# Kernel tuning notes

Hardware: AMD Instinct MI355X
Metric: run time of the kernel (lower is better)

The kernel has to match this reference:

```python
import jax, jax.numpy as jnp
import numpy as np

B, S, D, H = 2, 512, 1024, 8
DK = D // H
DFF = 4 * D
R = 51
SEP = 64


def setup_inputs() -> dict:
    key = jax.random.key(0)
    ks = jax.random.split(key, 12)
    def w(k, shape, scale=0.02):
        return jax.random.normal(k, shape, jnp.float32) * scale
    return {
        "x": jax.random.normal(ks[0], (B, S, D), jnp.float32),
        "relation": jax.random.randint(ks[1], (B, S, S), 0, R),
        "mask": jnp.ones((B, S, S), jnp.int32),
        "sep_id": SEP,
        "history_reg": jnp.ones((1,), jnp.float32),
        "Wq": w(ks[2], (D, D)), "bq": jnp.zeros((D,), jnp.float32),
        "Wk": w(ks[3], (D, D)), "bk": jnp.zeros((D,), jnp.float32),
        "Wv": w(ks[4], (D, D)), "bv": jnp.zeros((D,), jnp.float32),
        "Wo": w(ks[5], (D, D)), "bo": jnp.zeros((D,), jnp.float32),
        "rel_k_emb": w(ks[6], (R, DK)),
        "rel_v_emb": w(ks[7], (R, DK)),
        "ln1_g": jnp.ones((D,), jnp.float32), "ln1_b": jnp.zeros((D,), jnp.float32),
        "ln2_g": jnp.ones((D,), jnp.float32), "ln2_b": jnp.zeros((D,), jnp.float32),
        "W1": w(ks[8], (D, DFF)), "b1": jnp.zeros((DFF,), jnp.float32),
        "W2": w(ks[9], (DFF, D)), "b2": jnp.zeros((D,), jnp.float32),
    }


def _layer_norm(x, g, b, eps=1e-5):
    m = jnp.mean(x, axis=-1, keepdims=True)
    v = jnp.mean(jnp.square(x - m), axis=-1, keepdims=True)
    return (x - m) * jax.lax.rsqrt(v + eps) * g + b


def _forward(x, relation, mask, sep_id, history_reg, Wq, bq, Wk, bk, Wv, bv, Wo, bo,
             rel_k_emb, rel_v_emb, ln1_g, ln1_b, ln2_g, ln2_b, W1, b1, W2, b2):
    b, s, d = x.shape
    # relation-aware self-attention sublayer (pre-norm)
    h = _layer_norm(x, ln1_g, ln1_b)
    rk = rel_k_emb[relation]  # [B,S,S,DK]
    rv = rel_v_emb[relation]  # [B,S,S,DK]
    def proj(W, bias):
        return (h @ W + bias).reshape(b, s, H, DK).transpose(0, 2, 1, 3)  # [B,H,S,DK]
    q, k, v = proj(Wq, bq), proj(Wk, bk), proj(Wv, bv)
    scores = jnp.einsum("bhid,bhjd->bhij", q, k) + jnp.einsum("bhid,bijd->bhij", q, rk)
    scores = scores / jnp.sqrt(jnp.float32(DK))
    scores = jnp.where(mask[:, None, :, :] == 0, jnp.float32(-1e9), scores)
    attn = jax.nn.softmax(scores, axis=-1)  # [B,H,S,S]
    ctx = jnp.einsum("bhij,bhjd->bhid", attn, v) + jnp.einsum("bhij,bijd->bhid", attn, rv)
    ctx = ctx.transpose(0, 2, 1, 3).reshape(b, s, d)
    attn_out = ctx @ Wo + bo
    # history regularization loss: attention mass on history tokens (positions < sep_id)
    loss = history_reg[0] * jnp.mean(attn[:, :, :, :sep_id])
    x = x + attn_out
    # FFN sublayer (pre-norm)
    h2 = _layer_norm(x, ln2_g, ln2_b)
    ffn = jax.nn.relu(h2 @ W1 + b1) @ W2 + b2
    x = x + ffn
    return x, loss


def reference(x, relation, mask, sep_id, history_reg, Wq, bq, Wk, bk, Wv, bv, Wo, bo,
              rel_k_emb, rel_v_emb, ln1_g, ln1_b, ln2_g, ln2_b, W1, b1, W2, b2):
    return _forward(x, relation, mask, sep_id, history_reg, Wq, bq, Wk, bk, Wv, bv,
                    Wo, bo, rel_k_emb, rel_v_emb, ln1_g, ln1_b, ln2_g, ln2_b,
                    W1, b1, W2, b2)
```

## Files before the change

### kernel.cpp

```cpp
#include <hip/hip_runtime.h>
#include <hip/hip_bf16.h>

#define NB 2
#define NS 512
#define ND 1024
#define NH 8
#define NDK 128
#define NDFF 4096
#define RPAD 64
#define LDSC 640
#define BSROWS 1024
#define NBH 16

typedef __bf16 bf16x8 __attribute__((ext_vector_type(8)));
typedef __bf16 bf16x4 __attribute__((ext_vector_type(4)));
typedef float f32x4 __attribute__((ext_vector_type(4)));

#define BM 64
#define BN 64
#define BK 64

__device__ __forceinline__ void gload16(const void* g, void* l) {
    __builtin_amdgcn_global_load_lds(
        (const __attribute__((address_space(1))) void*)g,
        (__attribute__((address_space(3))) void*)l, 16, 0, 0);
}

__global__ __launch_bounds__(256, 4) void gemm64(
    const __bf16* __restrict__ A, const __bf16* __restrict__ Bt,
    const __bf16* __restrict__ Brel, __bf16* __restrict__ vt,
    const __bf16* __restrict__ arP, const __bf16* __restrict__ rvP,
    __bf16* __restrict__ ctxmP,
    float* __restrict__ Cf, __bf16* __restrict__ Cb,
    const float* __restrict__ bias,
    int Ksp, int lda, int ldb, int ldc,
    long sA, long sA2, int zdivA,
    long sB, long sB2, int zdivB,
    long sC, int nsplit, long sPart, int flags)
{
    __shared__ __bf16 As0[BM * BK];
    __shared__ __bf16 As1[BM * BK];
    __shared__ __bf16 Bs0[BN * BK];
    __shared__ __bf16 Bs1[BN * BK];

    const unsigned gx = gridDim.x, gy = gridDim.y;
    const unsigned n = gx * gy * gridDim.z;
    const unsigned o = blockIdx.x + gx * (blockIdx.y + gy * blockIdx.z);
    const unsigned q = n >> 3, r = n & 7, xcd = o & 7;
    const unsigned nl = (xcd < r ? xcd * (q + 1) : r * (q + 1) + (xcd - r) * q) + (o >> 3);
    const unsigned bx = nl % gx, tmp = nl / gx;
    const unsigned by = tmp % gy, bz = tmp / gy;

    const int z = bz;
    const int bh = z / nsplit, sp = z - bh * nsplit;
    const long kbase = (long)sp * Ksp;
    A  += (long)(bh / zdivA) * sA + (long)(bh % zdivA) * sA2 + kbase;
    Bt += (long)(bh / zdivB) * sB + (long)(bh % zdivB) * sB2 + kbase;
    const long cbase = (long)bh * sC + (long)sp * sPart;

    const int tM = by * BM, tN = bx * BN;
    const int t = threadIdx.x, lane = t & 63, w = t >> 6;
    const int wr = w >> 1, wc = w & 1;

    const __bf16* Bbase = Bt;
    int ldbx = ldb, tNB = tN;
    if ((flags & 4) && tN >= NS) { Bbase = Brel + kbase; ldbx = 128; tNB = tN - NS; }

    const int srow = lane >> 3;
    const int scolE = ((((lane & 7) << 4) ^ (srow << 4)) >> 1);

    const __bf16* gA = A + (long)(tM + srow) * lda + scolE;
    const __bf16* gB = Bbase + (long)(tNB + srow) * ldbx + scolE;

    f32x4 acc[2][2];
#pragma unroll
    for (int m = 0; m < 2; ++m)
#pragma unroll
        for (int nn = 0; nn < 2; ++nn)
#pragma unroll
            for (int j = 0; j < 4; ++j) acc[m][nn][j] = 0.f;

    const int r16 = lane & 15;
    const int kq = (lane >> 4) * 8;
    const int xorE = (r16 & 7) * 8;
    const int nt = Ksp / BK;

    auto STAGE = [&](__bf16* as, __bf16* bs, int k0) {
#pragma unroll
        for (int i = 0; i < 2; ++i) {
            const int rr = (w + i * 4) * 8;
            gload16(gA + (long)rr * lda + k0, (void*)&as[rr * BK]);
            gload16(gB + (long)rr * ldbx + k0, (void*)&bs[rr * BK]);
        }
    };
    auto COMPUTE = [&](const __bf16* as, const __bf16* bs) {
        __builtin_amdgcn_s_setprio(1);
#pragma unroll
        for (int ks = 0; ks < 2; ++ks) {
            bf16x8 af[2], bv[2];
#pragma unroll
            for (int m = 0; m < 2; ++m)
                af[m] = *(const bf16x8*)&as[(wr * 32 + m * 16 + r16) * BK + ((ks * 32 + kq) ^ xorE)];
#pragma unroll
            for (int nn = 0; nn < 2; ++nn)
                bv[nn] = *(const bf16x8*)&bs[(wc * 32 + nn * 16 + r16) * BK + ((ks * 32 + kq) ^ xorE)];
#pragma unroll
            for (int m = 0; m < 2; ++m)
#pragma unroll
                for (int nn = 0; nn < 2; ++nn)
                    acc[m][nn] = __builtin_amdgcn_mfma_f32_16x16x32_bf16(af[m], bv[nn], acc[m][nn], 0, 0, 0);
        }
        __builtin_amdgcn_s_setprio(0);
    };

    STAGE(As0, Bs0, 0);
    STAGE(As1, Bs1, BK);
    for (int tt = 0; tt < nt; tt += 2) {
        asm volatile("s_waitcnt vmcnt(4)\n\ts_barrier" ::: "memory");
        COMPUTE(As0, Bs0);
        asm volatile("s_waitcnt lgkmcnt(0)\n\ts_barrier" ::: "memory");
        const bool more = (tt + 2 < nt);
        if (more) {
            STAGE(As0, Bs0, (tt + 2) * BK);
            asm volatile("s_waitcnt vmcnt(4)\n\ts_barrier" ::: "memory");
        } else {
            asm volatile("s_waitcnt vmcnt(0)\n\ts_barrier" ::: "memory");
        }
        COMPUTE(As1, Bs1);
        asm volatile("s_waitcnt lgkmcnt(0)\n\ts_barrier" ::: "memory");
        if (more) STAGE(As1, Bs1, (tt + 3) * BK);
    }

    if (flags & 16) {
        const int b = bh >> 3, h = bh & 7;
#pragma unroll
        for (int nn = 0; nn < 2; ++nn) {
            const int gc = tN + wc * 32 + nn * 16 + (lane & 15);
            bf16x8 rv[8];
#pragma unroll
            for (int qq = 0; qq < 8; ++qq)
                rv[qq] = ((const bf16x8*)&rvP[(long)gc * RPAD])[qq];
#pragma unroll
            for (int m = 0; m < 2; ++m) {
                const int gr0 = tM + wr * 32 + m * 16 + (lane >> 4) * 4;
#pragma unroll
                for (int j = 0; j < 4; ++j) {
                    const int row = gr0 + j;
                    const bf16x8* ar8 = (const bf16x8*)&arP[((long)bh * NS + row) * RPAD];
                    float d = 0.f;
#pragma unroll
                    for (int qq = 0; qq < 8; ++qq) {
                        const bf16x8 a = ar8[qq], vv = rv[qq];
#pragma unroll
                        for (int e = 0; e < 8; ++e) d += (float)a[e] * (float)vv[e];
                    }
                    ctxmP[((long)(b * NS + row)) * ND + h * NDK + gc] =
                        (__bf16)(acc[m][nn][j] + d);
                }
            }
        }
        return;
    }

    const bool relu = (flags & 1) != 0;
    const bool vmode = (flags & 8) && (tN >= 2 * ND);
#pragma unroll
    for (int m = 0; m < 2; ++m) {
        const int gr0 = tM + wr * 32 + m * 16 + (lane >> 4) * 4;
#pragma unroll
        for (int nn = 0; nn < 2; ++nn) {
            const int gc = tN + wc * 32 + nn * 16 + (lane & 15);
            const float bb = bias ? bias[gc] : 0.f;
            if (vmode) {
                const int hd = gc - 2 * ND;
                const int b = gr0 >> 9, i = gr0 & 511;
                bf16x4 ov;
#pragma unroll
                for (int j = 0; j < 4; ++j) ov[j] = (__bf16)(acc[m][nn][j] + bb);
                *(bf16x4*)&vt[(((long)b * NH + (hd >> 7)) * NDK + (hd & 127)) * NS + i] = ov;
            } else {
#pragma unroll
                for (int j = 0; j < 4; ++j) {
                    float v = acc[m][nn][j] + bb;
                    if (relu) v = fmaxf(v, 0.f);
                    const long idx = cbase + (long)(gr0 + j) * ldc + gc;
                    if (Cb) Cb[idx] = (__bf16)v;
                    else Cf[idx] = v;
                }
            }
        }
    }
}

__global__ void prep_weights(
    const float* __restrict__ Wq, const float* __restrict__ Wk,
    const float* __restrict__ Wv, const float* __restrict__ Wo,
    const float* __restrict__ W1, const float* __restrict__ W2,
    const float* __restrict__ relv,
    const float* __restrict__ bq, const float* __restrict__ bk,
    const float* __restrict__ bv, const float* __restrict__ relk,
    const float* __restrict__ x, const float* __restrict__ ln1g,
    const float* __restrict__ ln1b,
    __bf16* __restrict__ WqkvT, __bf16* __restrict__ WoT,
    __bf16* __restrict__ W1T, __bf16* __restrict__ W2T,
    __bf16* __restrict__ relvT, float* __restrict__ biasqkv,
    __bf16* __restrict__ relkT, __bf16* __restrict__ h1, int R)
{
    const int tile = blockIdx.x;
    const int t = threadIdx.y * 32 + threadIdx.x;

    if (tile >= 12372) {
        const long row = tile - 12372;
        const float* xr = x + row * ND;
        float4 v = reinterpret_cast<const float4*>(xr)[t];
        float s = v.x + v.y + v.z + v.w;
        float s2 = v.x * v.x + v.y * v.y + v.z * v.z + v.w * v.w;
#pragma unroll
        for (int o = 32; o > 0; o >>= 1) {
            s += __shfl_xor(s, o, 64);
            s2 += __shfl_xor(s2, o, 64);
        }
        __shared__ float red[8];
        const int lane = t & 63, wv = t >> 6;
        if (lane == 0) { red[wv] = s; red[4 + wv] = s2; }
        __syncthreads();
        s = red[0] + red[1] + red[2] + red[3];
        s2 = red[4] + red[5] + red[6] + red[7];
        const float mean = s * (1.f / ND);
        const float var = s2 * (1.f / ND) - mean * mean;
        const float rs = rsqrtf(var + 1e-5f);
        const float xv[4] = {v.x, v.y, v.z, v.w};
        bf16x4 o;
#pragma unroll
        for (int j = 0; j < 4; ++j) {
            const int c = t * 4 + j;
            o[j] = (__bf16)((xv[j] - mean) * rs * ln1g[c] + ln1b[c]);
        }
        *(bf16x4*)&h1[row * ND + t * 4] = o;
        return;
    }
    if (tile >= 12296) {
        const int ft = (tile - 12296) * 256 + t;
        if (ft < ND) biasqkv[ft] = bq[ft];
        else if (ft < 2 * ND) biasqkv[ft] = bk[ft - ND];
        else if (ft < 3 * ND) biasqkv[ft] = bv[ft - 2 * ND];
        else {
            const int idx = ft - 3 * ND;
            if (idx < 128 * NDK) {
                const int r = idx / NDK;
                relkT[idx] = (r < R) ? (__bf16)relk[idx] : (__bf16)0.f;
            }
        }
        return;
    }
    const float* src; __bf16* dst;
    int rows_in, cols_in, ldo, kx, ny;
    if (tile < 4096) {
        const int m = tile >> 10, r = tile & 1023;
        kx = r & 31; ny = r >> 5;
        rows_in = 1024; cols_in = 1024; ldo = 1024;
        src = m == 0 ? Wq : m == 1 ? Wk : m == 2 ? Wv : Wo;
        dst = m == 3 ? WoT : WqkvT + (size_t)m * 1024 * 1024;
    } else if (tile < 8192) {
        const int r = tile - 4096;
        kx = r & 31; ny = r >> 5;
        rows_in = 1024; cols_in = 4096; ldo = 1024; src = W1; dst = W1T;
    } else if (tile < 12288) {
        const int r = tile - 8192;
        kx = r & 127; ny = r >> 7;
        rows_in = 4096; cols_in = 1024; ldo = 4096; src = W2; dst = W2T;
    } else {
        const int r = tile - 12288;
        kx = r & 1; ny = r >> 1;
        rows_in = R; cols_in = 128; ldo = 64; src = relv; dst = relvT;
    }

    __shared__ float tl[32][33];
    const int k0 = kx * 32, n0 = ny * 32;
    const int tx = threadIdx.x, ty = threadIdx.y;
#pragma unroll
    for (int dy = 0; dy < 32; dy += 8) {
        const int k = k0 + ty + dy, nn = n0 + tx;
        tl[ty + dy][tx] = (k < rows_in && nn < cols_in) ? src[(long)k * cols_in + nn] : 0.f;
    }
    __syncthreads();
#pragma unroll
    for (int dy = 0; dy < 32; dy += 8) {
        const int nn = n0 + ty + dy, k = k0 + tx;
        if (nn < cols_in && k < ldo) dst[(long)nn * ldo + k] = (__bf16)tl[tx][ty + dy];
    }
}

__global__ __launch_bounds__(256) void softmax_rel(
    const __bf16* __restrict__ scores,
    const int* __restrict__ relation, const int* __restrict__ mask,
    __bf16* __restrict__ attn, __bf16* __restrict__ attnR,
    float* __restrict__ loss_part, const int* __restrict__ sep_p)
{
    const int i = blockIdx.x, b = blockIdx.y;
    const int t = threadIdx.x;
    const int* rrow = relation + ((long)b * NS + i) * NS;
    const int* mrow = mask + ((long)b * NS + i) * NS;
    const int r0 = rrow[t], r1 = rrow[t + 256];
    const int m0 = mrow[t], m1 = mrow[t + 256];
    const int sep = *sep_p;
    const int lane = t & 63, wv = t >> 6;

    __shared__ float qrl[RPAD];
    __shared__ float bins[RPAD];
    __shared__ float red[4];

    const float sc = 0.088388347648318447f;
    float lsum = 0.f;

#pragma unroll 1
    for (int h = 0; h < NH; ++h) {
        const long bh = (long)(b * NH + h);
        const __bf16* srow = scores + (bh * NS + i) * LDSC;
        __bf16* arow = attn + (bh * NS + i) * NS;
        __bf16* aRrow = attnR + (bh * NS + i) * RPAD;

        if (t < RPAD) { qrl[t] = (float)srow[NS + t]; bins[t] = 0.f; }
        __syncthreads();

        float v0 = ((float)srow[t] + qrl[r0]) * sc;
        float v1 = ((float)srow[t + 256] + qrl[r1]) * sc;
        if (m0 == 0) v0 = -1e9f;
        if (m1 == 0) v1 = -1e9f;

        float mx = fmaxf(v0, v1);
#pragma unroll
        for (int o = 32; o > 0; o >>= 1) mx = fmaxf(mx, __shfl_xor(mx, o, 64));
        if (lane == 0) red[wv] = mx;
        __syncthreads();
        mx = fmaxf(fmaxf(red[0], red[1]), fmaxf(red[2], red[3]));
        __syncthreads();

        const float e0 = __expf(v0 - mx), e1 = __expf(v1 - mx);
        float sm = e0 + e1;
#pragma unroll
        for (int o = 32; o > 0; o >>= 1) sm += __shfl_xor(sm, o, 64);
        if (lane == 0) red[wv] = sm;
        __syncthreads();
        sm = red[0] + red[1] + red[2] + red[3];

        const float inv = 1.f / sm;
        const float a0 = e0 * inv, a1 = e1 * inv;
        arow[t] = (__bf16)a0;
        arow[t + 256] = (__bf16)a1;
        atomicAdd(&bins[r0], a0);
        atomicAdd(&bins[r1], a1);
        if (t < sep) lsum += a0;
        if (t + 256 < sep) lsum += a1;
        __syncthreads();
        if (t < RPAD) aRrow[t] = (__bf16)bins[t];
        __syncthreads();
    }

#pragma unroll
    for (int o = 32; o > 0; o >>= 1) lsum += __shfl_xor(lsum, o, 64);
    if (lane == 0) red[wv] = lsum;
    __syncthreads();
    if (t == 0) loss_part[(long)b * NS + i] = red[0] + red[1] + red[2] + red[3];
}

__global__ __launch_bounds__(256) void wo_reduce_ln(
    const float* __restrict__ P, const float* __restrict__ x,
    const float* __restrict__ bo, const float* __restrict__ g,
    const float* __restrict__ bb, float* __restrict__ out,
    __bf16* __restrict__ h2)
{
    const int row = blockIdx.x;
    const int t = threadIdx.x;
    const long i4 = (long)row * 256 + t;
    const long sP = (long)BSROWS * ND / 4;
    const float4* P4 = (const float4*)P;
    float4 s = P4[i4];
    const float4 t1 = P4[i4 + sP];
    s.x += t1.x; s.y += t1.y; s.z += t1.z; s.w += t1.w;
    const int col = t * 4;
    const float4 xv = ((const float4*)x)[i4];
    const float4 bv = *(const float4*)&bo[col];
    float4 o;
    o.x = s.x + xv.x + bv.x; o.y = s.y + xv.y + bv.y;
    o.z = s.z + xv.z + bv.z; o.w = s.w + xv.w + bv.w;
    ((float4*)out)[i4] = o;

    float sum = o.x + o.y + o.z + o.w;
    float sum2 = o.x * o.x + o.y * o.y + o.z * o.z + o.w * o.w;
#pragma unroll
    for (int of = 32; of > 0; of >>= 1) {
        sum += __shfl_xor(sum, of, 64);
        sum2 += __shfl_xor(sum2, of, 64);
    }
    __shared__ float red[8];
    const int lane = t & 63, wv = t >> 6;
    if (lane == 0) { red[wv] = sum; red[4 + wv] = sum2; }
    __syncthreads();
    sum = red[0] + red[1] + red[2] + red[3];
    sum2 = red[4] + red[5] + red[6] + red[7];
    const float mean = sum * (1.f / ND);
    const float var = sum2 * (1.f / ND) - mean * mean;
    const float rs = rsqrtf(var + 1e-5f);
    const float ov[4] = {o.x, o.y, o.z, o.w};
    bf16x4 hb;
#pragma unroll
    for (int j = 0; j < 4; ++j)
        hb[j] = (__bf16)((ov[j] - mean) * rs * g[col + j] + bb[col + j]);
    *(bf16x4*)&h2[(long)row * ND + col] = hb;
}

__global__ __launch_bounds__(256) void ffn2_reduce(
    const float* __restrict__ P, const float* __restrict__ b2, float* __restrict__ out,
    const float* __restrict__ loss_part, const float* __restrict__ hist,
    const int* __restrict__ sep_p, float* __restrict__ out_loss)
{
    const int i4 = blockIdx.x * 256 + threadIdx.x;
    const long sP = (long)BSROWS * ND / 4;
    const float4* P4 = (const float4*)P;
    float4 s = P4[i4];
    const float4 t1 = P4[i4 + sP];
    s.x += t1.x; s.y += t1.y; s.z += t1.z; s.w += t1.w;
    const int col = (i4 * 4) & (ND - 1);
    const float4 bv = *(const float4*)&b2[col];
    float4 o = ((float4*)out)[i4];
    o.x += s.x + bv.x; o.y += s.y + bv.y;
    o.z += s.z + bv.z; o.w += s.w + bv.w;
    ((float4*)out)[i4] = o;

    if (blockIdx.x == 0) {
        const int t = threadIdx.x;
        const float4 v = ((const float4*)loss_part)[t];
        float ls = v.x + v.y + v.z + v.w;
#pragma unroll
        for (int of = 32; of > 0; of >>= 1) ls += __shfl_xor(ls, of, 64);
        __shared__ float red[4];
        if ((t & 63) == 0) red[t >> 6] = ls;
        __syncthreads();
        if (t == 0) {
            const int sep = *sep_p;
            const float total = red[0] + red[1] + red[2] + red[3];
            const float denom = (float)NB * NH * NS * (float)(sep > 0 ? sep : 1);
            out_loss[0] = (sep > 0) ? hist[0] * total / denom : 0.f;
        }
    }
}

static inline int cdiv(int a, int b) { return (a + b - 1) / b; }

extern "C" void kernel_launch(void* const* d_in, const int* in_sizes, int n_in,
                              void* d_out, int out_size, void* d_ws, size_t ws_size,
                              hipStream_t stream)
{
    const float* x      = (const float*)d_in[0];
    const int* relation = (const int*)d_in[1];
    const int* mask     = (const int*)d_in[2];
    const int* sep_p    = (const int*)d_in[3];
    const float* hist   = (const float*)d_in[4];
    const float* Wq = (const float*)d_in[5],  *bq = (const float*)d_in[6];
    const float* Wk = (const float*)d_in[7],  *bk = (const float*)d_in[8];
    const float* Wv = (const float*)d_in[9],  *bv = (const float*)d_in[10];
    const float* Wo = (const float*)d_in[11], *bo = (const float*)d_in[12];
    const float* relk = (const float*)d_in[13];
    const float* relv = (const float*)d_in[14];
    const float* ln1g = (const float*)d_in[15], *ln1b = (const float*)d_in[16];
    const float* ln2g = (const float*)d_in[17], *ln2b = (const float*)d_in[18];
    const float* W1 = (const float*)d_in[19], *b1 = (const float*)d_in[20];
    const float* W2 = (const float*)d_in[21], *b2 = (const float*)d_in[22];
    const int R = in_sizes[13] / NDK;

    float* out = (float*)d_out;
    float* out_loss = out + (long)BSROWS * ND;

    char* p = (char*)d_ws;
    auto alloc = [&](size_t bytes) -> void* {
        void* r = (void*)p;
        p += (bytes + 255) & ~(size_t)255;
        return r;
    };
    __bf16* WqkvT   = (__bf16*)alloc((size_t)3 * ND * ND * 2);
    __bf16* WoT     = (__bf16*)alloc((size_t)ND * ND * 2);
    __bf16* W1T     = (__bf16*)alloc((size_t)NDFF * ND * 2);
    __bf16* W2T     = (__bf16*)alloc((size_t)ND * NDFF * 2);
    __bf16* relkT   = (__bf16*)alloc((size_t)128 * NDK * 2);
    __bf16* relvT   = (__bf16*)alloc((size_t)NDK * RPAD * 2);
    float*  biasqkv = (float*)alloc((size_t)3 * ND * 4);
    __bf16* h1      = (__bf16*)alloc((size_t)BSROWS * ND * 2);
    __bf16* qkvb    = (__bf16*)alloc((size_t)BSROWS * 3 * ND * 2);
    __bf16* vt      = (__bf16*)alloc((size_t)NBH * NDK * NS * 2);
    __bf16* attnb   = (__bf16*)alloc((size_t)NBH * NS * NS * 2);
    __bf16* attnR   = (__bf16*)alloc((size_t)NBH * NS * RPAD * 2);
    __bf16* ctxm    = (__bf16*)alloc((size_t)BSROWS * ND * 2);
    __bf16* h2      = (__bf16*)alloc((size_t)BSROWS * ND * 2);
    __bf16* F1      = (__bf16*)alloc((size_t)BSROWS * NDFF * 2);
    float*  loss_part = (float*)alloc((size_t)NB * NS * 4);
    float*  arena   = (float*)alloc((size_t)64 * 1024 * 1024);
    __bf16* scoresb = (__bf16*)arena;
    float* woPart   = arena;
    float* f2Part   = arena + (size_t)2 * 1024 * 1024;

    const dim3 tb(32, 8);
    prep_weights<<<13396, tb, 0, stream>>>(Wq, Wk, Wv, Wo, W1, W2, relv,
                                           bq, bk, bv, relk, x, ln1g, ln1b,
                                           WqkvT, WoT, W1T, W2T, relvT,
                                           biasqkv, relkT, h1, R);

    gemm64<<<dim3(48, 16, 1), 256, 0, stream>>>(
        h1, WqkvT, nullptr, vt, nullptr, nullptr, nullptr,
        nullptr, qkvb, biasqkv,
        ND, ND, ND, 3 * ND,
        0, 0, 1, 0, 0, 1, 0, 1, 0, 8);

    gemm64<<<dim3(10, 8, NBH), 256, 0, stream>>>(
        qkvb, qkvb + ND, relkT, nullptr, nullptr, nullptr, nullptr,
        nullptr, scoresb, nullptr,
        NDK, 3 * ND, 3 * ND, LDSC,
        (long)NS * 3 * ND, NDK, NH,
        (long)NS * 3 * ND, NDK, NH,
        (long)NS * LDSC, 1, 0, 4);

    softmax_rel<<<dim3(NS, NB), 256, 0, stream>>>(
        scoresb, relation, mask, attnb, attnR, loss_part, sep_p);

    gemm64<<<dim3(2, 8, NBH), 256, 0, stream>>>(
        attnb, vt, nullptr, nullptr, attnR, relvT, ctxm,
        nullptr, nullptr, nullptr,
        NS, NS, NS, NDK,
        (long)NS * NS, 0, 1,
        (long)NDK * NS, 0, 1,
        0, 1, 0, 16);

    gemm64<<<dim3(16, 16, 2), 256, 0, stream>>>(
        ctxm, WoT, nullptr, nullptr, nullptr, nullptr, nullptr,
        woPart, nullptr, nullptr,
        512, ND, ND, ND,
        0, 0, 1, 0, 0, 1,
        0, 2, (long)BSROWS * ND, 0);

    wo_reduce_ln<<<BSROWS, 256, 0, stream>>>(woPart, x, bo, ln2g, ln2b, out, h2);

    gemm64<<<dim3(64, 16, 1), 256, 0, stream>>>(
        h2, W1T, nullptr, nullptr, nullptr, nullptr, nullptr,
        nullptr, F1, b1,
        ND, ND, ND, NDFF,
        0, 0, 1, 0, 0, 1, 0, 1, 0, 1);

    gemm64<<<dim3(16, 16, 2), 256, 0, stream>>>(
        F1, W2T, nullptr, nullptr, nullptr, nullptr, nullptr,
        f2Part, nullptr, nullptr,
        2048, NDFF, NDFF, ND,
        0, 0, 1, 0, 0, 1,
        0, 2, (long)BSROWS * ND, 0);

    ffn2_reduce<<<1024, 256, 0, stream>>>(f2Part, b2, out,
                                          loss_part, hist, sep_p, out_loss);
}
```

Baseline: 159.2 us.

## Fuse relation-aware attention into one kernel per 16-query tile

Replaces the three-kernel attention path (QK+relK scores GEMM, softmax_rel, attn·V GEMM with relV epilogue) with a single attn_fused kernel. Each block holds a 16-row score tile in LDS, computes QK^T and q·relK with MFMA, applies softmax with relation bins and the history loss, then multiplies by V and relV directly. This removes the global round-trips of the bf16 scores and attention matrices and two launches. In exchange each block carries a large LDS footprint, which limits occupancy, and V is read straight from global memory rather than staged through LDS.

```diff
diff --git a/kernel.cpp b/kernel.cpp
--- a/kernel.cpp
+++ b/kernel.cpp
@@ -8,9 +8,10 @@
 #define NDK 128
 #define NDFF 4096
 #define RPAD 64
-#define LDSC 640
 #define BSROWS 1024
 #define NBH 16
+#define QT 16
+#define SLP 524
 
 typedef __bf16 bf16x8 __attribute__((ext_vector_type(8)));
 typedef __bf16 bf16x4 __attribute__((ext_vector_type(4)));
@@ -28,9 +29,7 @@
 
 __global__ __launch_bounds__(256, 4) void gemm64(
     const __bf16* __restrict__ A, const __bf16* __restrict__ Bt,
-    const __bf16* __restrict__ Brel, __bf16* __restrict__ vt,
-    const __bf16* __restrict__ arP, const __bf16* __restrict__ rvP,
-    __bf16* __restrict__ ctxmP,
+    __bf16* __restrict__ vt,
     float* __restrict__ Cf, __bf16* __restrict__ Cb,
     const float* __restrict__ bias,
     int Ksp, int lda, int ldb, int ldc,
@@ -62,15 +61,11 @@
     const int t = threadIdx.x, lane = t & 63, w = t >> 6;
     const int wr = w >> 1, wc = w & 1;
 
-    const __bf16* Bbase = Bt;
-    int ldbx = ldb, tNB = tN;
-    if ((flags & 4) && tN >= NS) { Bbase = Brel + kbase; ldbx = 128; tNB = tN - NS; }
-
     const int srow = lane >> 3;
     const int scolE = ((((lane & 7) << 4) ^ (srow << 4)) >> 1);
 
     const __bf16* gA = A + (long)(tM + srow) * lda + scolE;
-    const __bf16* gB = Bbase + (long)(tNB + srow) * ldbx + scolE;
+    const __bf16* gB = Bt + (long)(tN + srow) * ldb + scolE;
 
     f32x4 acc[2][2];
 #pragma unroll
@@ -90,7 +85,7 @@
         for (int i = 0; i < 2; ++i) {
             const int rr = (w + i * 4) * 8;
             gload16(gA + (long)rr * lda + k0, (void*)&as[rr * BK]);
-            gload16(gB + (long)rr * ldbx + k0, (void*)&bs[rr * BK]);
+            gload16(gB + (long)rr * ldb + k0, (void*)&bs[rr * BK]);
         }
     };
     auto COMPUTE = [&](const __bf16* as, const __bf16* bs) {
@@ -131,37 +126,6 @@
         if (more) STAGE(As1, Bs1, (tt + 3) * BK);
     }
 
-    if (flags & 16) {
-        const int b = bh >> 3, h = bh & 7;
-#pragma unroll
-        for (int nn = 0; nn < 2; ++nn) {
-            const int gc = tN + wc * 32 + nn * 16 + (lane & 15);
-            bf16x8 rv[8];
-#pragma unroll
-            for (int qq = 0; qq < 8; ++qq)
-                rv[qq] = ((const bf16x8*)&rvP[(long)gc * RPAD])[qq];
-#pragma unroll
-            for (int m = 0; m < 2; ++m) {
-                const int gr0 = tM + wr * 32 + m * 16 + (lane >> 4) * 4;
-#pragma unroll
-                for (int j = 0; j < 4; ++j) {
-                    const int row = gr0 + j;
-                    const bf16x8* ar8 = (const bf16x8*)&arP[((long)bh * NS + row) * RPAD];
-                    float d = 0.f;
-#pragma unroll
-                    for (int qq = 0; qq < 8; ++qq) {
-                        const bf16x8 a = ar8[qq], vv = rv[qq];
-#pragma unroll
-                        for (int e = 0; e < 8; ++e) d += (float)a[e] * (float)vv[e];
-                    }
-                    ctxmP[((long)(b * NS + row)) * ND + h * NDK + gc] =
-                        (__bf16)(acc[m][nn][j] + d);
-                }
-            }
-        }
-        return;
-    }
-
     const bool relu = (flags & 1) != 0;
     const bool vmode = (flags & 8) && (tN >= 2 * ND);
 #pragma unroll
@@ -190,6 +154,180 @@
             }
         }
     }
+}
+
+__global__ __launch_bounds__(256, 2) void attn_fused(
+    const __bf16* __restrict__ qkvb, const __bf16* __restrict__ vt,
+    const __bf16* __restrict__ relkT, const __bf16* __restrict__ relvT,
+    const int* __restrict__ relation, const int* __restrict__ mask,
+    __bf16* __restrict__ ctxm, float* __restrict__ loss_part,
+    const int* __restrict__ sep_p)
+{
+    __shared__ float Sl[QT * SLP];
+    __shared__ __bf16 Ks0[64 * NDK];
+    __shared__ __bf16 Ks1[64 * NDK];
+    __shared__ float qrl[QT][RPAD];
+    __shared__ float bins[QT][68];
+    __shared__ float redl[4];
+
+    const unsigned o = blockIdx.x + 32u * blockIdx.y;
+    const unsigned nl = (o & 7) * 64u + (o >> 3);
+    const int qt = nl & 31, bh = nl >> 5;
+    const int b = bh >> 3, h = bh & 7;
+    const int i0 = qt * QT;
+
+    const int t = threadIdx.x, lane = t & 63, w = t >> 6;
+    const int r16 = lane & 15;
+    const int kq = (lane >> 4) * 8;
+    const int xorE = (r16 & 7) * 8;
+    const int sep = *sep_p;
+
+    bf16x8 qf[4];
+    {
+        const __bf16* qrow = qkvb + ((long)(b * NS + i0 + r16)) * (3 * ND) + h * NDK;
+#pragma unroll
+        for (int ks = 0; ks < 4; ++ks)
+            qf[ks] = *(const bf16x8*)(qrow + ks * 32 + kq);
+    }
+
+    {
+        f32x4 a;
+#pragma unroll
+        for (int j = 0; j < 4; ++j) a[j] = 0.f;
+#pragma unroll
+        for (int ks = 0; ks < 4; ++ks) {
+            const bf16x8 bfr = *(const bf16x8*)(relkT + (long)(w * 16 + r16) * NDK + ks * 32 + kq);
+            a = __builtin_amdgcn_mfma_f32_16x16x32_bf16(qf[ks], bfr, a, 0, 0, 0);
+        }
+#pragma unroll
+        for (int j = 0; j < 4; ++j)
+            qrl[(lane >> 4) * 4 + j][w * 16 + (lane & 15)] = a[j];
+    }
+    for (int idx = t; idx < QT * 68; idx += 256) ((float*)bins)[idx] = 0.f;
+
+    auto KSTAGE = [&](__bf16* ksb, int kv0) {
+#pragma unroll
+        for (int ii = 0; ii < 4; ++ii) {
+            const int Lc = (w * 4 + ii) * 64 + lane;
+            const int j = Lc >> 4, cc = Lc & 15;
+            gload16(qkvb + ((long)(b * NS + kv0 + j)) * (3 * ND) + ND + h * NDK + ((cc ^ (j & 7)) << 3),
+                    (void*)&ksb[(w * 4 + ii) * 512]);
+        }
+    };
+    auto SCOMP = [&](const __bf16* ksb, int kv0) {
+        f32x4 s;
+#pragma unroll
+        for (int j = 0; j < 4; ++j) s[j] = 0.f;
+#pragma unroll
+        for (int ks = 0; ks < 4; ++ks) {
+            const bf16x8 bfr = *(const bf16x8*)&ksb[(w * 16 + r16) * NDK + ((ks * 32 + kq) ^ xorE)];
+            s = __builtin_amdgcn_mfma_f32_16x16x32_bf16(qf[ks], bfr, s, 0, 0, 0);
+        }
+        const int colb = kv0 + w * 16 + (lane & 15);
+#pragma unroll
+        for (int j = 0; j < 4; ++j)
+            Sl[((lane >> 4) * 4 + j) * SLP + colb] = s[j];
+    };
+
+    KSTAGE(Ks0, 0);
+    KSTAGE(Ks1, 64);
+    for (int tt = 0; tt < 8; tt += 2) {
+        asm volatile("s_waitcnt vmcnt(4)\n\ts_barrier" ::: "memory");
+        SCOMP(Ks0, tt * 64);
+        asm volatile("s_waitcnt lgkmcnt(0)\n\ts_barrier" ::: "memory");
+        const bool more = (tt + 2 < 8);
+        if (more) {
+            KSTAGE(Ks0, (tt + 2) * 64);
+            asm volatile("s_waitcnt vmcnt(4)\n\ts_barrier" ::: "memory");
+        } else {
+            asm volatile("s_waitcnt vmcnt(0)\n\ts_barrier" ::: "memory");
+        }
+        SCOMP(Ks1, (tt + 1) * 64);
+        asm volatile("s_waitcnt lgkmcnt(0)\n\ts_barrier" ::: "memory");
+        if (more) KSTAGE(Ks1, (tt + 3) * 64);
+    }
+
+    const float sc = 0.088388347648318447f;
+    float lsum = 0.f;
+#pragma unroll 1
+    for (int rr = 0; rr < 4; ++rr) {
+        const int row = w * 4 + rr;
+        const int* relrow = relation + ((long)(b * NS + i0 + row)) * NS;
+        const int* mrow = mask + ((long)(b * NS + i0 + row)) * NS;
+        float v[8]; int rl[8];
+        float mx = -1e30f;
+#pragma unroll
+        for (int c = 0; c < 8; ++c) {
+            const int j = lane + c * 64;
+            const float s = Sl[row * SLP + j];
+            rl[c] = relrow[j];
+            float vv = (s + qrl[row][rl[c]]) * sc;
+            if (mrow[j] == 0) vv = -1e9f;
+            v[c] = vv;
+            mx = fmaxf(mx, vv);
+        }
+#pragma unroll
+        for (int of = 32; of > 0; of >>= 1) mx = fmaxf(mx, __shfl_xor(mx, of, 64));
+        float sm = 0.f;
+#pragma unroll
+        for (int c = 0; c < 8; ++c) { v[c] = __expf(v[c] - mx); sm += v[c]; }
+#pragma unroll
+        for (int of = 32; of > 0; of >>= 1) sm += __shfl_xor(sm, of, 64);
+        const float inv = 1.f / sm;
+#pragma unroll
+        for (int c = 0; c < 8; ++c) {
+            const float a = v[c] * inv;
+            Sl[row * SLP + lane + c * 64] = a;
+            atomicAdd(&bins[row][rl[c]], a);
+            if (lane + c * 64 < sep) lsum += a;
+        }
+    }
+#pragma unroll
+    for (int of = 32; of > 0; of >>= 1) lsum += __shfl_xor(lsum, of, 64);
+    if (lane == 0) redl[w] = lsum;
+    __syncthreads();
+    if (t == 0) loss_part[bh * 32 + qt] = redl[0] + redl[1] + redl[2] + redl[3];
+
+    f32x4 oacc[2];
+#pragma unroll
+    for (int nn = 0; nn < 2; ++nn)
+#pragma unroll
+        for (int j = 0; j < 4; ++j) oacc[nn][j] = 0.f;
+
+#pragma unroll
+    for (int kc = 0; kc < 16; ++kc) {
+        const float4 a0 = *(const float4*)&Sl[r16 * SLP + kc * 32 + kq];
+        const float4 a1 = *(const float4*)&Sl[r16 * SLP + kc * 32 + kq + 4];
+        bf16x8 af;
+        af[0] = (__bf16)a0.x; af[1] = (__bf16)a0.y; af[2] = (__bf16)a0.z; af[3] = (__bf16)a0.w;
+        af[4] = (__bf16)a1.x; af[5] = (__bf16)a1.y; af[6] = (__bf16)a1.z; af[7] = (__bf16)a1.w;
+#pragma unroll
+        for (int nn = 0; nn < 2; ++nn) {
+            const bf16x8 bfr = *(const bf16x8*)(vt + ((long)bh * NDK + w * 32 + nn * 16 + r16) * NS + kc * 32 + kq);
+            oacc[nn] = __builtin_amdgcn_mfma_f32_16x16x32_bf16(af, bfr, oacc[nn], 0, 0, 0);
+        }
+    }
+#pragma unroll
+    for (int kc = 0; kc < 2; ++kc) {
+        const float4 b0 = *(const float4*)&bins[r16][kc * 32 + kq];
+        const float4 b1 = *(const float4*)&bins[r16][kc * 32 + kq + 4];
+        bf16x8 af;
+        af[0] = (__bf16)b0.x; af[1] = (__bf16)b0.y; af[2] = (__bf16)b0.z; af[3] = (__bf16)b0.w;
+        af[4] = (__bf16)b1.x; af[5] = (__bf16)b1.y; af[6] = (__bf16)b1.z; af[7] = (__bf16)b1.w;
+#pragma unroll
+        for (int nn = 0; nn < 2; ++nn) {
+            const bf16x8 bfr = *(const bf16x8*)(relvT + (long)(w * 32 + nn * 16 + r16) * RPAD + kc * 32 + kq);
+            oacc[nn] = __builtin_amdgcn_mfma_f32_16x16x32_bf16(af, bfr, oacc[nn], 0, 0, 0);
+        }
+    }
+#pragma unroll
+    for (int nn = 0; nn < 2; ++nn)
+#pragma unroll
+        for (int j = 0; j < 4; ++j) {
+            const int row = (lane >> 4) * 4 + j;
+            ctxm[((long)(b * NS + i0 + row)) * ND + h * NDK + w * 32 + nn * 16 + (lane & 15)] =
+                (__bf16)oacc[nn][j];
+        }
 }
 
 __global__ void prep_weights(
@@ -289,79 +427,6 @@
         const int nn = n0 + ty + dy, k = k0 + tx;
         if (nn < cols_in && k < ldo) dst[(long)nn * ldo + k] = (__bf16)tl[tx][ty + dy];
     }
-}
-
-__global__ __launch_bounds__(256) void softmax_rel(
-    const __bf16* __restrict__ scores,
-    const int* __restrict__ relation, const int* __restrict__ mask,
-    __bf16* __restrict__ attn, __bf16* __restrict__ attnR,
-    float* __restrict__ loss_part, const int* __restrict__ sep_p)
-{
-    const int i = blockIdx.x, b = blockIdx.y;
-    const int t = threadIdx.x;
-    const int* rrow = relation + ((long)b * NS + i) * NS;
-    const int* mrow = mask + ((long)b * NS + i) * NS;
-    const int r0 = rrow[t], r1 = rrow[t + 256];
-    const int m0 = mrow[t], m1 = mrow[t + 256];
-    const int sep = *sep_p;
-    const int lane = t & 63, wv = t >> 6;
-
-    __shared__ float qrl[RPAD];
-    __shared__ float bins[RPAD];
-    __shared__ float red[4];
-
-    const float sc = 0.088388347648318447f;
-    float lsum = 0.f;
-
-#pragma unroll 1
-    for (int h = 0; h < NH; ++h) {
-        const long bh = (long)(b * NH + h);
-        const __bf16* srow = scores + (bh * NS + i) * LDSC;
-        __bf16* arow = attn + (bh * NS + i) * NS;
-        __bf16* aRrow = attnR + (bh * NS + i) * RPAD;
-
-        if (t < RPAD) { qrl[t] = (float)srow[NS + t]; bins[t] = 0.f; }
-        __syncthreads();
-
-        float v0 = ((float)srow[t] + qrl[r0]) * sc;
-        float v1 = ((float)srow[t + 256] + qrl[r1]) * sc;
-        if (m0 == 0) v0 = -1e9f;
-        if (m1 == 0) v1 = -1e9f;
-
-        float mx = fmaxf(v0, v1);
-#pragma unroll
-        for (int o = 32; o > 0; o >>= 1) mx = fmaxf(mx, __shfl_xor(mx, o, 64));
-        if (lane == 0) red[wv] = mx;
-        __syncthreads();
-        mx = fmaxf(fmaxf(red[0], red[1]), fmaxf(red[2], red[3]));
-        __syncthreads();
-
-        const float e0 = __expf(v0 - mx), e1 = __expf(v1 - mx);
-        float sm = e0 + e1;
-#pragma unroll
-        for (int o = 32; o > 0; o >>= 1) sm += __shfl_xor(sm, o, 64);
-        if (lane == 0) red[wv] = sm;
-        __syncthreads();
-        sm = red[0] + red[1] + red[2] + red[3];
-
-        const float inv = 1.f / sm;
-        const float a0 = e0 * inv, a1 = e1 * inv;
-        arow[t] = (__bf16)a0;
-        arow[t + 256] = (__bf16)a1;
-        atomicAdd(&bins[r0], a0);
-        atomicAdd(&bins[r1], a1);
-        if (t < sep) lsum += a0;
-        if (t + 256 < sep) lsum += a1;
-        __syncthreads();
-        if (t < RPAD) aRrow[t] = (__bf16)bins[t];
-        __syncthreads();
-    }
-
-#pragma unroll
-    for (int o = 32; o > 0; o >>= 1) lsum += __shfl_xor(lsum, o, 64);
-    if (lane == 0) red[wv] = lsum;
-    __syncthreads();
-    if (t == 0) loss_part[(long)b * NS + i] = red[0] + red[1] + red[2] + red[3];
 }
 
 __global__ __launch_bounds__(256) void wo_reduce_ln(
@@ -430,8 +495,11 @@
 
     if (blockIdx.x == 0) {
         const int t = threadIdx.x;
-        const float4 v = ((const float4*)loss_part)[t];
-        float ls = v.x + v.y + v.z + v.w;
+        float ls = 0.f;
+        if (t < 128) {
+            const float4 v = ((const float4*)loss_part)[t];
+            ls = v.x + v.y + v.z + v.w;
+        }
 #pragma unroll
         for (int of = 32; of > 0; of >>= 1) ls += __shfl_xor(ls, of, 64);
         __shared__ float red[4];
@@ -445,8 +513,6 @@
         }
     }
 }
-
-static inline int cdiv(int a, int b) { return (a + b - 1) / b; }
 
 extern "C" void kernel_launch(void* const* d_in, const int* in_sizes, int n_in,
                               void* d_out, int out_size, void* d_ws, size_t ws_size,
@@ -488,14 +554,11 @@
     __bf16* h1      = (__bf16*)alloc((size_t)BSROWS * ND * 2);
     __bf16* qkvb    = (__bf16*)alloc((size_t)BSROWS * 3 * ND * 2);
     __bf16* vt      = (__bf16*)alloc((size_t)NBH * NDK * NS * 2);
-    __bf16* attnb   = (__bf16*)alloc((size_t)NBH * NS * NS * 2);
-    __bf16* attnR   = (__bf16*)alloc((size_t)NBH * NS * RPAD * 2);
     __bf16* ctxm    = (__bf16*)alloc((size_t)BSROWS * ND * 2);
     __bf16* h2      = (__bf16*)alloc((size_t)BSROWS * ND * 2);
     __bf16* F1      = (__bf16*)alloc((size_t)BSROWS * NDFF * 2);
-    float*  loss_part = (float*)alloc((size_t)NB * NS * 4);
-    float*  arena   = (float*)alloc((size_t)64 * 1024 * 1024);
-    __bf16* scoresb = (__bf16*)arena;
+    float*  loss_part = (float*)alloc((size_t)512 * 4);
+    float*  arena   = (float*)alloc((size_t)16 * 1024 * 1024);
     float* woPart   = arena;
     float* f2Part   = arena + (size_t)2 * 1024 * 1024;
 
@@ -506,33 +569,15 @@
                                            biasqkv, relkT, h1, R);
 
     gemm64<<<dim3(48, 16, 1), 256, 0, stream>>>(
-        h1, WqkvT, nullptr, vt, nullptr, nullptr, nullptr,
-        nullptr, qkvb, biasqkv,
+        h1, WqkvT, vt, nullptr, qkvb, biasqkv,
         ND, ND, ND, 3 * ND,
         0, 0, 1, 0, 0, 1, 0, 1, 0, 8);
 
-    gemm64<<<dim3(10, 8, NBH), 256, 0, stream>>>(
-        qkvb, qkvb + ND, relkT, nullptr, nullptr, nullptr, nullptr,
-        nullptr, scoresb, nullptr,
-        NDK, 3 * ND, 3 * ND, LDSC,
-        (long)NS * 3 * ND, NDK, NH,
-        (long)NS * 3 * ND, NDK, NH,
-        (long)NS * LDSC, 1, 0, 4);
-
-    softmax_rel<<<dim3(NS, NB), 256, 0, stream>>>(
-        scoresb, relation, mask, attnb, attnR, loss_part, sep_p);
-
-    gemm64<<<dim3(2, 8, NBH), 256, 0, stream>>>(
-        attnb, vt, nullptr, nullptr, attnR, relvT, ctxm,
-        nullptr, nullptr, nullptr,
-        NS, NS, NS, NDK,
-        (long)NS * NS, 0, 1,
-        (long)NDK * NS, 0, 1,
-        0, 1, 0, 16);
+    attn_fused<<<dim3(32, 16), 256, 0, stream>>>(
+        qkvb, vt, relkT, relvT, relation, mask, ctxm, loss_part, sep_p);
 
     gemm64<<<dim3(16, 16, 2), 256, 0, stream>>>(
-        ctxm, WoT, nullptr, nullptr, nullptr, nullptr, nullptr,
-        woPart, nullptr, nullptr,
+        ctxm, WoT, nullptr, woPart, nullptr, nullptr,
         512, ND, ND, ND,
         0, 0, 1, 0, 0, 1,
         0, 2, (long)BSROWS * ND, 0);
@@ -540,14 +585,12 @@
     wo_reduce_ln<<<BSROWS, 256, 0, stream>>>(woPart, x, bo, ln2g, ln2b, out, h2);
 
     gemm64<<<dim3(64, 16, 1), 256, 0, stream>>>(
-        h2, W1T, nullptr, nullptr, nullptr, nullptr, nullptr,
-        nullptr, F1, b1,
+        h2, W1T, nullptr, nullptr, F1, b1,
         ND, ND, ND, NDFF,
         0, 0, 1, 0, 0, 1, 0, 1, 0, 1);
 
     gemm64<<<dim3(16, 16, 2), 256, 0, stream>>>(
-        F1, W2T, nullptr, nullptr, nullptr, nullptr, nullptr,
-        f2Part, nullptr, nullptr,
+        F1, W2T, nullptr, f2Part, nullptr, nullptr,
         2048, NDFF, NDFF, ND,
         0, 0, 1, 0, 0, 1,
         0, 2, (long)BSROWS * ND, 0);
```

Result: faster. 131.4 us (median of 2 runs) (-17.4%).
